# Performance work log

Measured on AMD Instinct MI355X. Metric: run time of the kernel, lower is better.

Reference implementation:

```python
import jax, jax.numpy as jnp
import numpy as np

B, L, E, H = 2, 2048, 1024, 16
HD = E // H          # head_dim = 64
G = H // 4           # heads per kernel-size group = 4


def _dwconv(x, w, b):
    """Causal depthwise conv. x: (B, G, L, D); w: (D, k); b: (D,).
    Matches PadLeft(k-1) + Conv1d(D, D, k, groups=D): y[l] = sum_j w[:, j] * x[l - (k-1) + j] + b."""
    k = w.shape[-1]
    Lx = x.shape[2]
    xp = jnp.pad(x, ((0, 0), (0, 0), (k - 1, 0), (0, 0)))
    out = b
    for j in range(k):
        out = out + xp[:, :, j:j + Lx, :] * w[:, j]
    return out


def setup_inputs() -> dict:
    key = jax.random.key(0)
    ks = jax.random.split(key, 32)
    s = 0.02
    inp = {"x": jax.random.normal(ks[0], (B, L, E), jnp.float32)}
    for i, n in enumerate(["Wq", "Wk", "Wv", "Wo"]):
        inp[n] = jax.random.normal(ks[1 + i], (E, E), jnp.float32) * s
    inp["bo"] = jax.random.normal(ks[5], (E,), jnp.float32) * s
    i = 6
    for ksz in (3, 5, 7):
        for pfx in ("q", "k", "v"):
            inp[f"{pfx}{ksz}_w"] = jax.random.normal(ks[i], (HD, ksz), jnp.float32) * (1.0 / ksz)
            inp[f"{pfx}{ksz}_b"] = jax.random.normal(ks[i + 1], (HD,), jnp.float32) * s
            i += 2
    return inp


def reference(x, Wq, Wk, Wv, Wo, bo,
              q3_w, q3_b, k3_w, k3_b, v3_w, v3_b,
              q5_w, q5_b, k5_w, k5_b, v5_w, v5_b,
              q7_w, q7_b, k7_w, k7_b, v7_w, v7_b):
    b, l, _ = x.shape

    def split(t):  # (b, l, E) -> (b, 4, G, l, HD)
        return t.reshape(b, l, 4, G, HD).transpose(0, 2, 3, 1, 4)

    q = split(x @ Wq.T)
    k = split(x @ Wk.T)
    v = split(x @ Wv.T)

    # NOTE: faithful to source quirks -- k and v convs are applied to the
    # (already convolved) q group, not to k/v.
    q0, k0, v0 = q[:, 0], k[:, 0], v[:, 0]
    q1 = _dwconv(q[:, 1], q3_w, q3_b)
    k1 = _dwconv(q1, k3_w, k3_b)
    v1 = _dwconv(q1, v3_w, v3_b)
    q2 = _dwconv(q[:, 2], q5_w, q5_b)
    k2 = _dwconv(q2, k5_w, k5_b)
    v2 = _dwconv(q2, v5_w, v5_b)
    q3 = _dwconv(q[:, 3], q7_w, q7_b)
    k3 = _dwconv(q3, k7_w, k7_b)
    v3 = _dwconv(q3, v7_w, v7_b)

    Q = jnp.concatenate([q0, q1, q2, q3], axis=1)  # (b, H, l, HD)
    K = jnp.concatenate([k0, k1, k2, k3], axis=1)
    V = jnp.concatenate([v0, v1, v2, v3], axis=1)

    logit = jnp.einsum('bnid,bnjd->bnij', Q, K) * (HD ** -0.5)
    attn = jax.nn.softmax(logit, axis=-1)
    attn_out = jnp.einsum('bnij,bnjd->bnid', attn, V)

    # Source quirk: output uses rearranged V, discarding attn_out.
    out = V.transpose(0, 2, 1, 3).reshape(b, l, E)
    # keep the attention compute alive without changing the math
    out = out + 0.0 * attn_out.transpose(0, 2, 1, 3).reshape(b, l, E)
    return out @ Wo.T + bo
```

## Files before the change

### kernel.cpp

```cpp
#include <hip/hip_runtime.h>
#include <hip/hip_bf16.h>
#include <stdint.h>

#define L_SEQ 2048
#define MTOT  4096
#define EDIM  1024

typedef __attribute__((ext_vector_type(8))) short bf16x8;
typedef __attribute__((ext_vector_type(4))) float f32x4;
typedef __attribute__((ext_vector_type(16))) float f32x16;
typedef __attribute__((ext_vector_type(4))) float float4v;
typedef __attribute__((ext_vector_type(4))) unsigned short us4;

__device__ __forceinline__ unsigned short f2b(float f) {
    union { float f; unsigned u; } v; v.f = f;
    return (unsigned short)((v.u + 0x7FFFu + ((v.u >> 16) & 1u)) >> 16);
}
__device__ __forceinline__ float b2f(unsigned short h) {
    union { unsigned u; float f; } v; v.u = ((unsigned)h) << 16;
    return v.f;
}
__device__ __forceinline__ unsigned cvtpk(float lo, float hi) {
    unsigned r;
    asm("v_cvt_pk_bf16_f32 %0, %1, %2" : "=v"(r) : "v"(lo), "v"(hi));
    return r;
}
__device__ __forceinline__ void lds16(const void* g, void* l) {
    __builtin_amdgcn_global_load_lds((const __attribute__((address_space(1))) void*)g,
                                     (__attribute__((address_space(3))) void*)l, 16, 0, 0);
}

__global__ __launch_bounds__(256) void wprep_kernel(
    const float* __restrict__ Wq, const float* __restrict__ Wv,
    const float* __restrict__ Wo,
    unsigned short* __restrict__ W1b, unsigned short* __restrict__ Wob,
    const float* __restrict__ q3w, const float* __restrict__ q3b,
    const float* __restrict__ v3w, const float* __restrict__ v3b,
    const float* __restrict__ q5w, const float* __restrict__ q5b,
    const float* __restrict__ v5w, const float* __restrict__ v5b,
    const float* __restrict__ q7w, const float* __restrict__ q7b,
    const float* __restrict__ v7w, const float* __restrict__ v7b,
    float* __restrict__ H, float* __restrict__ Beff, float* __restrict__ Corr)
{
    if (blockIdx.x >= 2048) {
        int ch = (blockIdx.x - 2048) * 256 + threadIdx.x;
        int g = ch >> 8, d = ch & 63, k = 3 + 2 * g;
        const float* qw = (g == 0) ? q3w : (g == 1) ? q5w : q7w;
        const float* qb = (g == 0) ? q3b : (g == 1) ? q5b : q7b;
        const float* vw = (g == 0) ? v3w : (g == 1) ? v5w : v7w;
        const float* vb = (g == 0) ? v3b : (g == 1) ? v5b : v7b;

        float hq[7], hv[7];
        for (int i = 0; i < 7; ++i) { hq[i] = 0.f; hv[i] = 0.f; }
        for (int i = 0; i < k; ++i) {
            hq[i] = qw[d * k + (k - 1 - i)];
            hv[i] = vw[d * k + (k - 1 - i)];
        }
        float h[13];
        for (int i = 0; i < 13; ++i) h[i] = 0.f;
        for (int a = 0; a < 7; ++a)
            for (int b = 0; b < 7; ++b)
                h[a + b] += hq[a] * hv[b];
        for (int i = 0; i < 13; ++i) H[i * 768 + ch] = h[i];

        float sv = 0.f;
        for (int j = 0; j < k; ++j) sv += vw[d * k + j];
        Beff[ch] = qb[d] * sv + vb[d];

        for (int l = 0; l < 6; ++l) {
            float s2 = 0.f;
            for (int i = l + 1; i < 7; ++i) s2 += hv[i];
            Corr[l * 768 + ch] = qb[d] * s2;
        }
        return;
    }
    const int WQ = (EDIM * EDIM) / 4;
    int i = blockIdx.x * 256 + threadIdx.x;
    const float* src;
    unsigned short* dst;
    int j;
    if (i < WQ) {
        j = i * 4;
        int row = j >> 10;
        src = (row < 256) ? Wv : Wq;
        dst = W1b;
    } else {
        j = (i - WQ) * 4; src = Wo; dst = Wob;
    }
    float4v v = *(const float4v*)(src + j);
    us4 o;
    o[0] = f2b(v[0]); o[1] = f2b(v[1]); o[2] = f2b(v[2]); o[3] = f2b(v[3]);
    *(us4*)(dst + j) = o;
}

template <int TA, int OUT_MODE>
__global__ __launch_bounds__(512, 2) void gemm_f(
    const float* __restrict__ Af,
    const unsigned short* __restrict__ Ab0, const unsigned short* __restrict__ Ab1,
    int tsplit,
    const unsigned short* __restrict__ BT,
    unsigned short* __restrict__ Cb, float* __restrict__ Cf,
    const float* __restrict__ bias)
{
    constexpr int ABUF = TA ? 49152 : 32768;
    constexpr int ABYT = TA ? 32768 : 16384;
    __shared__ uint8_t sh[3 * ABUF];

    int orig = blockIdx.y * 8 + blockIdx.x;
    int wg   = (orig & 7) * 32 + (orig >> 3);
    const int m0 = (wg >> 3) * 128, n0 = (wg & 7) * 128;

    const int tid  = threadIdx.x;
    const int wid  = tid >> 6;
    const int lane = tid & 63;
    const int wr   = wid >> 2;
    const int wc   = (wid >> 1) & 1;
    const int kh   = wid & 1;
    const int l31  = lane & 31, hi = lane >> 5;

    f32x16 acc[2][2] = {};

    auto stage = [&](int buf, int t) {
        uint8_t* Abase = sh + buf * ABUF;
        uint8_t* Bbase = Abase + ABYT;
        if (TA) {
            const float* Asrc = Af + (size_t)m0 * EDIM + t * 64;
#pragma unroll
            for (int j = 0; j < 4; ++j) {
                int slot = j * 512 + tid;
                int row = slot >> 4, c = (slot & 15) ^ (row & 15);
                lds16(Asrc + (size_t)row * EDIM + c * 4,
                      Abase + j * 8192 + wid * 1024);
            }
        } else {
            const unsigned short* Asrc =
                (t < tsplit ? Ab0 : Ab1) + (size_t)m0 * EDIM + t * 64;
#pragma unroll
            for (int j = 0; j < 2; ++j) {
                int slot = j * 512 + tid;
                int row = slot >> 3, c = (slot & 7) ^ (row & 7);
                lds16(Asrc + (size_t)row * EDIM + c * 8,
                      Abase + j * 8192 + wid * 1024);
            }
        }
        const unsigned short* Bsrc = BT + (size_t)n0 * EDIM + t * 64;
#pragma unroll
        for (int j = 0; j < 2; ++j) {
            int slot = j * 512 + tid;
            int row = slot >> 3, c = (slot & 7) ^ (row & 7);
            lds16(Bsrc + (size_t)row * EDIM + c * 8,
                  Bbase + j * 8192 + wid * 1024);
        }
    };

    auto compute = [&](int buf) {
        const uint8_t* Abase = sh + buf * ABUF;
        const unsigned short* bs = (const unsigned short*)(Abase + ABYT);
#pragma unroll
        for (int s = 0; s < 2; ++s) {
            bf16x8 a[2], b[2];
#pragma unroll
            for (int mi = 0; mi < 2; ++mi) {
                int row = wr * 64 + mi * 32 + l31;
                if (TA) {
                    const float* as = (const float*)Abase;
                    int c0 = kh * 8 + s * 4 + hi * 2;
                    f32x4 lo = *(const f32x4*)(as + row * 64 + ((c0 ^ (row & 15)) * 4));
                    f32x4 h4 = *(const f32x4*)(as + row * 64 + (((c0 + 1) ^ (row & 15)) * 4));
                    union { unsigned u[4]; bf16x8 v; } fu;
                    fu.u[0] = cvtpk(lo[0], lo[1]); fu.u[1] = cvtpk(lo[2], lo[3]);
                    fu.u[2] = cvtpk(h4[0], h4[1]); fu.u[3] = cvtpk(h4[2], h4[3]);
                    a[mi] = fu.v;
                } else {
                    const unsigned short* as = (const unsigned short*)Abase;
                    int cg = kh * 4 + s * 2 + hi;
                    a[mi] = *(const bf16x8*)(as + row * 64 + ((cg ^ (row & 7)) * 8));
                }
            }
#pragma unroll
            for (int ni = 0; ni < 2; ++ni) {
                int row = wc * 64 + ni * 32 + l31;
                int cg = kh * 4 + s * 2 + hi;
                b[ni] = *(const bf16x8*)(bs + row * 64 + ((cg ^ (row & 7)) * 8));
            }
#pragma unroll
            for (int mi = 0; mi < 2; ++mi)
#pragma unroll
                for (int ni = 0; ni < 2; ++ni)
                    acc[mi][ni] = __builtin_amdgcn_mfma_f32_32x32x16_bf16(a[mi], b[ni], acc[mi][ni], 0, 0, 0);
        }
    };

    const int NT = EDIM >> 6;
    stage(0, 0);
    stage(1, 1);
    if (TA) asm volatile("s_waitcnt vmcnt(6)" ::: "memory");
    else    asm volatile("s_waitcnt vmcnt(4)" ::: "memory");
    __builtin_amdgcn_s_barrier();
    asm volatile("" ::: "memory");

    for (int t = 0; t < NT; ++t) {
        if (t + 2 < NT) stage((t + 2) % 3, t + 2);
        compute(t % 3);
        if (t + 1 < NT) {
            if (t + 2 < NT) {
                if (TA) asm volatile("s_waitcnt vmcnt(6)" ::: "memory");
                else    asm volatile("s_waitcnt vmcnt(4)" ::: "memory");
            } else {
                asm volatile("s_waitcnt vmcnt(0)" ::: "memory");
            }
            __builtin_amdgcn_s_barrier();
            asm volatile("" ::: "memory");
        }
    }

    __syncthreads();
    float* Mg = (float*)sh;
    const int mgbase = (wr * 2 + wc) * 4096;
    if (kh) {
#pragma unroll
        for (int mi = 0; mi < 2; ++mi)
#pragma unroll
            for (int ni = 0; ni < 2; ++ni) {
                int col = ni * 32 + l31;
#pragma unroll
                for (int q = 0; q < 4; ++q) {
                    int grp = mi * 8 + 2 * q + hi;
                    int adr = mgbase + col * 64 + (((grp) ^ (col & 15)) << 2);
                    f32x4 v;
                    v[0] = acc[mi][ni][q * 4 + 0]; v[1] = acc[mi][ni][q * 4 + 1];
                    v[2] = acc[mi][ni][q * 4 + 2]; v[3] = acc[mi][ni][q * 4 + 3];
                    *(f32x4*)(Mg + adr) = v;
                }
            }
    }
    __syncthreads();
    if (!kh) {
#pragma unroll
        for (int mi = 0; mi < 2; ++mi) {
#pragma unroll
            for (int ni = 0; ni < 2; ++ni) {
                int col = ni * 32 + l31;
                int gcol = n0 + wc * 64 + col;
#pragma unroll
                for (int q = 0; q < 4; ++q) {
                    int grp = mi * 8 + 2 * q + hi;
                    int adr = mgbase + col * 64 + (((grp) ^ (col & 15)) << 2);
                    f32x4 p = *(const f32x4*)(Mg + adr);
                    int rowb = m0 + wr * 64 + mi * 32 + 8 * q + 4 * hi;
#pragma unroll
                    for (int j = 0; j < 4; ++j) {
                        float v = acc[mi][ni][q * 4 + j] + p[j];
                        if (OUT_MODE == 0) {
                            Cb[(size_t)(rowb + j) * EDIM + gcol] = f2b(v);
                        } else {
                            Cf[(size_t)(rowb + j) * EDIM + gcol] = v + bias[gcol];
                        }
                    }
                }
            }
        }
    }
}

__global__ __launch_bounds__(256) void conv_kernel(
    const unsigned short* __restrict__ T, unsigned short* __restrict__ V,
    const float* __restrict__ H, const float* __restrict__ Beff,
    const float* __restrict__ Corr)
{
    unsigned w  = blockIdx.x * 256 + threadIdx.x;
    unsigned rp = w / 192u;
    int c4 = (int)(w - rp * 192u);
    int m  = (int)rp * 2;
    int ch = c4 * 4;
    int e0 = 256 + ch;
    const unsigned short* tp = T + (size_t)m * EDIM + e0;
    unsigned short*       vp = V + (size_t)m * EDIM + e0;
    int l  = m & (L_SEQ - 1);
    float4v b4 = *(const float4v*)(Beff + ch);
    float4v acc0 = b4, acc1 = b4;

    {
        float4v h = *(const float4v*)(H + ch);
        us4 t = *(const us4*)(tp + EDIM);
        acc1[0] += h[0] * b2f(t[0]); acc1[1] += h[1] * b2f(t[1]);
        acc1[2] += h[2] * b2f(t[2]); acc1[3] += h[3] * b2f(t[3]);
    }
    int ni = (l < 12) ? l : 12;
    for (int i = 0; i <= ni; ++i) {
        us4 t = *(const us4*)(tp - (size_t)i * EDIM);
        float4v h0 = *(const float4v*)(H + i * 768 + ch);
        acc0[0] += h0[0] * b2f(t[0]); acc0[1] += h0[1] * b2f(t[1]);
        acc0[2] += h0[2] * b2f(t[2]); acc0[3] += h0[3] * b2f(t[3]);
        if (i < 12) {
            float4v h1 = *(const float4v*)(H + (i + 1) * 768 + ch);
            acc1[0] += h1[0] * b2f(t[0]); acc1[1] += h1[1] * b2f(t[1]);
            acc1[2] += h1[2] * b2f(t[2]); acc1[3] += h1[3] * b2f(t[3]);
        }
    }
    if (l < 6) {
        float4v c = *(const float4v*)(Corr + l * 768 + ch);
        acc0[0] -= c[0]; acc0[1] -= c[1]; acc0[2] -= c[2]; acc0[3] -= c[3];
    }
    if (l + 1 < 6) {
        float4v c = *(const float4v*)(Corr + (l + 1) * 768 + ch);
        acc1[0] -= c[0]; acc1[1] -= c[1]; acc1[2] -= c[2]; acc1[3] -= c[3];
    }
    us4 o0, o1;
    o0[0] = f2b(acc0[0]); o0[1] = f2b(acc0[1]); o0[2] = f2b(acc0[2]); o0[3] = f2b(acc0[3]);
    o1[0] = f2b(acc1[0]); o1[1] = f2b(acc1[1]); o1[2] = f2b(acc1[2]); o1[3] = f2b(acc1[3]);
    *(us4*)vp = o0;
    *(us4*)(vp + EDIM) = o1;
}

extern "C" void kernel_launch(void* const* d_in, const int* in_sizes, int n_in,
                              void* d_out, int out_size, void* d_ws, size_t ws_size,
                              hipStream_t stream)
{
    const float* x  = (const float*)d_in[0];
    const float* Wq = (const float*)d_in[1];
    const float* Wv = (const float*)d_in[3];
    const float* Wo = (const float*)d_in[4];
    const float* bo = (const float*)d_in[5];

    uint8_t* ws = (uint8_t*)d_ws;
    unsigned short* W1b = (unsigned short*)(ws);
    unsigned short* Wob = (unsigned short*)(ws + (2u  << 20));
    unsigned short* T   = (unsigned short*)(ws + (4u  << 20));
    unsigned short* V   = (unsigned short*)(ws + (12u << 20));
    float* H    = (float*)(ws + (20u << 20));
    float* Beff = (float*)(ws + (20u << 20) + (64u << 10));
    float* Corr = (float*)(ws + (20u << 20) + (96u << 10));

    wprep_kernel<<<2051, 256, 0, stream>>>(
        Wq, Wv, Wo, W1b, Wob,
        (const float*)d_in[6],  (const float*)d_in[7],
        (const float*)d_in[10], (const float*)d_in[11],
        (const float*)d_in[12], (const float*)d_in[13],
        (const float*)d_in[16], (const float*)d_in[17],
        (const float*)d_in[18], (const float*)d_in[19],
        (const float*)d_in[22], (const float*)d_in[23],
        H, Beff, Corr);

    dim3 gg(EDIM / 128, MTOT / 128);
    gemm_f<1, 0><<<gg, 512, 0, stream>>>(x, nullptr, nullptr, 0,
                                         W1b, T, nullptr, nullptr);

    conv_kernel<<<1536, 256, 0, stream>>>(T, V, H, Beff, Corr);

    gemm_f<0, 1><<<gg, 512, 0, stream>>>(nullptr, T, V, 4,
                                         Wob, nullptr, (float*)d_out, bo);
}
```

Baseline: 53.78 us.

## Halve GEMM K-tile to shrink LDS and raise occupancy, deepen bf16 pipeline

```diff
diff --git a/kernel.cpp b/kernel.cpp
--- a/kernel.cpp
+++ b/kernel.cpp
@@ -94,7 +94,7 @@
 }
 
 template <int TA, int OUT_MODE>
-__global__ __launch_bounds__(512, 2) void gemm_f(
+__global__ __launch_bounds__(512, 4) void gemm_f(
     const float* __restrict__ Af,
     const unsigned short* __restrict__ Ab0, const unsigned short* __restrict__ Ab1,
     int tsplit,
@@ -102,9 +102,11 @@
     unsigned short* __restrict__ Cb, float* __restrict__ Cf,
     const float* __restrict__ bias)
 {
-    constexpr int ABUF = TA ? 49152 : 32768;
-    constexpr int ABYT = TA ? 32768 : 16384;
-    __shared__ uint8_t sh[3 * ABUF];
+    constexpr int ABYT = TA ? 16384 : 8192;
+    constexpr int BBYT = 8192;
+    constexpr int BUF  = ABYT + BBYT;
+    constexpr int NBUF = TA ? 3 : 4;
+    __shared__ uint8_t sh[NBUF * BUF];
 
     int orig = blockIdx.y * 8 + blockIdx.x;
     int wg   = (orig & 7) * 32 + (orig >> 3);
@@ -121,93 +123,85 @@
     f32x16 acc[2][2] = {};
 
     auto stage = [&](int buf, int t) {
-        uint8_t* Abase = sh + buf * ABUF;
+        uint8_t* Abase = sh + buf * BUF;
         uint8_t* Bbase = Abase + ABYT;
         if (TA) {
-            const float* Asrc = Af + (size_t)m0 * EDIM + t * 64;
-#pragma unroll
-            for (int j = 0; j < 4; ++j) {
+            const float* Asrc = Af + (size_t)m0 * EDIM + t * 32;
+#pragma unroll
+            for (int j = 0; j < 2; ++j) {
                 int slot = j * 512 + tid;
-                int row = slot >> 4, c = (slot & 15) ^ (row & 15);
+                int row = slot >> 3, c = (slot & 7) ^ (row & 7);
                 lds16(Asrc + (size_t)row * EDIM + c * 4,
                       Abase + j * 8192 + wid * 1024);
             }
         } else {
             const unsigned short* Asrc =
-                (t < tsplit ? Ab0 : Ab1) + (size_t)m0 * EDIM + t * 64;
-#pragma unroll
-            for (int j = 0; j < 2; ++j) {
-                int slot = j * 512 + tid;
-                int row = slot >> 3, c = (slot & 7) ^ (row & 7);
-                lds16(Asrc + (size_t)row * EDIM + c * 8,
-                      Abase + j * 8192 + wid * 1024);
+                (t < tsplit ? Ab0 : Ab1) + (size_t)m0 * EDIM + t * 32;
+            int row = tid >> 2, c = (tid & 3) ^ (row & 3);
+            lds16(Asrc + (size_t)row * EDIM + c * 8, Abase + wid * 1024);
+        }
+        const unsigned short* Bsrc = BT + (size_t)n0 * EDIM + t * 32;
+        int row = tid >> 2, c = (tid & 3) ^ (row & 3);
+        lds16(Bsrc + (size_t)row * EDIM + c * 8, Bbase + wid * 1024);
+    };
+
+    auto compute = [&](int buf) {
+        const uint8_t* Abase = sh + buf * BUF;
+        const unsigned short* bs = (const unsigned short*)(Abase + ABYT);
+        bf16x8 a[2], b[2];
+#pragma unroll
+        for (int mi = 0; mi < 2; ++mi) {
+            int row = wr * 64 + mi * 32 + l31;
+            if (TA) {
+                const float* as = (const float*)Abase;
+                int c0 = kh * 4 + hi * 2;
+                f32x4 lo = *(const f32x4*)(as + row * 32 + ((c0 ^ (row & 7)) * 4));
+                f32x4 h4 = *(const f32x4*)(as + row * 32 + (((c0 + 1) ^ (row & 7)) * 4));
+                union { unsigned u[4]; bf16x8 v; } fu;
+                fu.u[0] = cvtpk(lo[0], lo[1]); fu.u[1] = cvtpk(lo[2], lo[3]);
+                fu.u[2] = cvtpk(h4[0], h4[1]); fu.u[3] = cvtpk(h4[2], h4[3]);
+                a[mi] = fu.v;
+            } else {
+                const unsigned short* as = (const unsigned short*)Abase;
+                int cg = kh * 2 + hi;
+                a[mi] = *(const bf16x8*)(as + row * 32 + ((cg ^ (row & 3)) * 8));
             }
         }
-        const unsigned short* Bsrc = BT + (size_t)n0 * EDIM + t * 64;
-#pragma unroll
-        for (int j = 0; j < 2; ++j) {
-            int slot = j * 512 + tid;
-            int row = slot >> 3, c = (slot & 7) ^ (row & 7);
-            lds16(Bsrc + (size_t)row * EDIM + c * 8,
-                  Bbase + j * 8192 + wid * 1024);
-        }
+#pragma unroll
+        for (int ni = 0; ni < 2; ++ni) {
+            int row = wc * 64 + ni * 32 + l31;
+            int cg = kh * 2 + hi;
+            b[ni] = *(const bf16x8*)(bs + row * 32 + ((cg ^ (row & 3)) * 8));
+        }
+#pragma unroll
+        for (int mi = 0; mi < 2; ++mi)
+#pragma unroll
+            for (int ni = 0; ni < 2; ++ni)
+                acc[mi][ni] = __builtin_amdgcn_mfma_f32_32x32x16_bf16(a[mi], b[ni], acc[mi][ni], 0, 0, 0);
     };
 
-    auto compute = [&](int buf) {
-        const uint8_t* Abase = sh + buf * ABUF;
-        const unsigned short* bs = (const unsigned short*)(Abase + ABYT);
-#pragma unroll
-        for (int s = 0; s < 2; ++s) {
-            bf16x8 a[2], b[2];
-#pragma unroll
-            for (int mi = 0; mi < 2; ++mi) {
-                int row = wr * 64 + mi * 32 + l31;
-                if (TA) {
-                    const float* as = (const float*)Abase;
-                    int c0 = kh * 8 + s * 4 + hi * 2;
-                    f32x4 lo = *(const f32x4*)(as + row * 64 + ((c0 ^ (row & 15)) * 4));
-                    f32x4 h4 = *(const f32x4*)(as + row * 64 + (((c0 + 1) ^ (row & 15)) * 4));
-                    union { unsigned u[4]; bf16x8 v; } fu;
-                    fu.u[0] = cvtpk(lo[0], lo[1]); fu.u[1] = cvtpk(lo[2], lo[3]);
-                    fu.u[2] = cvtpk(h4[0], h4[1]); fu.u[3] = cvtpk(h4[2], h4[3]);
-                    a[mi] = fu.v;
-                } else {
-                    const unsigned short* as = (const unsigned short*)Abase;
-                    int cg = kh * 4 + s * 2 + hi;
-                    a[mi] = *(const bf16x8*)(as + row * 64 + ((cg ^ (row & 7)) * 8));
-                }
-            }
-#pragma unroll
-            for (int ni = 0; ni < 2; ++ni) {
-                int row = wc * 64 + ni * 32 + l31;
-                int cg = kh * 4 + s * 2 + hi;
-                b[ni] = *(const bf16x8*)(bs + row * 64 + ((cg ^ (row & 7)) * 8));
-            }
-#pragma unroll
-            for (int mi = 0; mi < 2; ++mi)
-#pragma unroll
-                for (int ni = 0; ni < 2; ++ni)
-                    acc[mi][ni] = __builtin_amdgcn_mfma_f32_32x32x16_bf16(a[mi], b[ni], acc[mi][ni], 0, 0, 0);
-        }
-    };
-
-    const int NT = EDIM >> 6;
+    const int NT = EDIM >> 5;
+    constexpr int LPT = TA ? 3 : 2;
     stage(0, 0);
     stage(1, 1);
-    if (TA) asm volatile("s_waitcnt vmcnt(6)" ::: "memory");
+    if (!TA) stage(2, 2);
+    if (TA) asm volatile("s_waitcnt vmcnt(3)" ::: "memory");
     else    asm volatile("s_waitcnt vmcnt(4)" ::: "memory");
     __builtin_amdgcn_s_barrier();
     asm volatile("" ::: "memory");
 
     for (int t = 0; t < NT; ++t) {
-        if (t + 2 < NT) stage((t + 2) % 3, t + 2);
-        compute(t % 3);
+        constexpr int D = NBUF - 1;
+        if (t + D < NT) stage((t + D) % NBUF, t + D);
+        compute(t % NBUF);
         if (t + 1 < NT) {
-            if (t + 2 < NT) {
-                if (TA) asm volatile("s_waitcnt vmcnt(6)" ::: "memory");
-                else    asm volatile("s_waitcnt vmcnt(4)" ::: "memory");
+            if (TA) {
+                if (t + 2 < NT) asm volatile("s_waitcnt vmcnt(3)" ::: "memory");
+                else            asm volatile("s_waitcnt vmcnt(0)" ::: "memory");
             } else {
-                asm volatile("s_waitcnt vmcnt(0)" ::: "memory");
+                if (t + 3 < NT)      asm volatile("s_waitcnt vmcnt(4)" ::: "memory");
+                else if (t + 2 < NT) asm volatile("s_waitcnt vmcnt(2)" ::: "memory");
+                else                 asm volatile("s_waitcnt vmcnt(0)" ::: "memory");
             }
             __builtin_amdgcn_s_barrier();
             asm volatile("" ::: "memory");
@@ -216,50 +210,54 @@
 
     __syncthreads();
     float* Mg = (float*)sh;
-    const int mgbase = (wr * 2 + wc) * 4096;
-    if (kh) {
-#pragma unroll
-        for (int mi = 0; mi < 2; ++mi)
-#pragma unroll
-            for (int ni = 0; ni < 2; ++ni) {
-                int col = ni * 32 + l31;
-#pragma unroll
-                for (int q = 0; q < 4; ++q) {
-                    int grp = mi * 8 + 2 * q + hi;
-                    int adr = mgbase + col * 64 + (((grp) ^ (col & 15)) << 2);
-                    f32x4 v;
-                    v[0] = acc[mi][ni][q * 4 + 0]; v[1] = acc[mi][ni][q * 4 + 1];
-                    v[2] = acc[mi][ni][q * 4 + 2]; v[3] = acc[mi][ni][q * 4 + 3];
-                    *(f32x4*)(Mg + adr) = v;
+#pragma unroll
+    for (int p = 0; p < 2; ++p) {
+        const int mgbase = wc * 4096;
+        if (kh && wr == p) {
+#pragma unroll
+            for (int mi = 0; mi < 2; ++mi)
+#pragma unroll
+                for (int ni = 0; ni < 2; ++ni) {
+                    int col = ni * 32 + l31;
+#pragma unroll
+                    for (int q = 0; q < 4; ++q) {
+                        int grp = mi * 8 + 2 * q + hi;
+                        int adr = mgbase + col * 64 + (((grp) ^ (col & 15)) << 2);
+                        f32x4 v;
+                        v[0] = acc[mi][ni][q * 4 + 0]; v[1] = acc[mi][ni][q * 4 + 1];
+                        v[2] = acc[mi][ni][q * 4 + 2]; v[3] = acc[mi][ni][q * 4 + 3];
+                        *(f32x4*)(Mg + adr) = v;
+                    }
                 }
-            }
-    }
-    __syncthreads();
-    if (!kh) {
-#pragma unroll
-        for (int mi = 0; mi < 2; ++mi) {
-#pragma unroll
-            for (int ni = 0; ni < 2; ++ni) {
-                int col = ni * 32 + l31;
-                int gcol = n0 + wc * 64 + col;
-#pragma unroll
-                for (int q = 0; q < 4; ++q) {
-                    int grp = mi * 8 + 2 * q + hi;
-                    int adr = mgbase + col * 64 + (((grp) ^ (col & 15)) << 2);
-                    f32x4 p = *(const f32x4*)(Mg + adr);
-                    int rowb = m0 + wr * 64 + mi * 32 + 8 * q + 4 * hi;
-#pragma unroll
-                    for (int j = 0; j < 4; ++j) {
-                        float v = acc[mi][ni][q * 4 + j] + p[j];
-                        if (OUT_MODE == 0) {
-                            Cb[(size_t)(rowb + j) * EDIM + gcol] = f2b(v);
-                        } else {
-                            Cf[(size_t)(rowb + j) * EDIM + gcol] = v + bias[gcol];
+        }
+        __syncthreads();
+        if (!kh && wr == p) {
+#pragma unroll
+            for (int mi = 0; mi < 2; ++mi) {
+#pragma unroll
+                for (int ni = 0; ni < 2; ++ni) {
+                    int col = ni * 32 + l31;
+                    int gcol = n0 + wc * 64 + col;
+#pragma unroll
+                    for (int q = 0; q < 4; ++q) {
+                        int grp = mi * 8 + 2 * q + hi;
+                        int adr = mgbase + col * 64 + (((grp) ^ (col & 15)) << 2);
+                        f32x4 pp = *(const f32x4*)(Mg + adr);
+                        int rowb = m0 + wr * 64 + mi * 32 + 8 * q + 4 * hi;
+#pragma unroll
+                        for (int j = 0; j < 4; ++j) {
+                            float v = acc[mi][ni][q * 4 + j] + pp[j];
+                            if (OUT_MODE == 0) {
+                                Cb[(size_t)(rowb + j) * EDIM + gcol] = f2b(v);
+                            } else {
+                                Cf[(size_t)(rowb + j) * EDIM + gcol] = v + bias[gcol];
+                            }
                         }
                     }
                 }
             }
         }
+        __syncthreads();
     }
 }
 
@@ -348,6 +346,6 @@
 
     conv_kernel<<<1536, 256, 0, stream>>>(T, V, H, Beff, Corr);
 
-    gemm_f<0, 1><<<gg, 512, 0, stream>>>(nullptr, T, V, 4,
+    gemm_f<0, 1><<<gg, 512, 0, stream>>>(nullptr, T, V, 8,
                                          Wob, nullptr, (float*)d_out, bo);
 }
```

Measured after the change: 83.08 us. 54.5% more time.

## Move Wo bf16 conversion into conv kernel and deepen output GEMM pipeline

Applied to the files above, without the earlier changes.

```diff
diff --git a/kernel.cpp b/kernel.cpp
--- a/kernel.cpp
+++ b/kernel.cpp
@@ -32,8 +32,7 @@
 
 __global__ __launch_bounds__(256) void wprep_kernel(
     const float* __restrict__ Wq, const float* __restrict__ Wv,
-    const float* __restrict__ Wo,
-    unsigned short* __restrict__ W1b, unsigned short* __restrict__ Wob,
+    unsigned short* __restrict__ W1b,
     const float* __restrict__ q3w, const float* __restrict__ q3b,
     const float* __restrict__ v3w, const float* __restrict__ v3b,
     const float* __restrict__ q5w, const float* __restrict__ q5b,
@@ -42,8 +41,8 @@
     const float* __restrict__ v7w, const float* __restrict__ v7b,
     float* __restrict__ H, float* __restrict__ Beff, float* __restrict__ Corr)
 {
-    if (blockIdx.x >= 2048) {
-        int ch = (blockIdx.x - 2048) * 256 + threadIdx.x;
+    if (blockIdx.x >= 1024) {
+        int ch = (blockIdx.x - 1024) * 256 + threadIdx.x;
         int g = ch >> 8, d = ch & 63, k = 3 + 2 * g;
         const float* qw = (g == 0) ? q3w : (g == 1) ? q5w : q7w;
         const float* qb = (g == 0) ? q3b : (g == 1) ? q5b : q7b;
@@ -74,23 +73,13 @@
         }
         return;
     }
-    const int WQ = (EDIM * EDIM) / 4;
-    int i = blockIdx.x * 256 + threadIdx.x;
-    const float* src;
-    unsigned short* dst;
-    int j;
-    if (i < WQ) {
-        j = i * 4;
-        int row = j >> 10;
-        src = (row < 256) ? Wv : Wq;
-        dst = W1b;
-    } else {
-        j = (i - WQ) * 4; src = Wo; dst = Wob;
-    }
+    int j = (blockIdx.x * 256 + threadIdx.x) * 4;
+    int row = j >> 10;
+    const float* src = (row < 256) ? Wv : Wq;
     float4v v = *(const float4v*)(src + j);
     us4 o;
     o[0] = f2b(v[0]); o[1] = f2b(v[1]); o[2] = f2b(v[2]); o[3] = f2b(v[3]);
-    *(us4*)(dst + j) = o;
+    *(us4*)(W1b + j) = o;
 }
 
 template <int TA, int OUT_MODE>
@@ -104,7 +93,8 @@
 {
     constexpr int ABUF = TA ? 49152 : 32768;
     constexpr int ABYT = TA ? 32768 : 16384;
-    __shared__ uint8_t sh[3 * ABUF];
+    constexpr int NBUF = TA ? 3 : 4;
+    __shared__ uint8_t sh[NBUF * ABUF];
 
     int orig = blockIdx.y * 8 + blockIdx.x;
     int wg   = (orig & 7) * 32 + (orig >> 3);
@@ -194,20 +184,24 @@
     const int NT = EDIM >> 6;
     stage(0, 0);
     stage(1, 1);
+    if (!TA) stage(2, 2);
     if (TA) asm volatile("s_waitcnt vmcnt(6)" ::: "memory");
-    else    asm volatile("s_waitcnt vmcnt(4)" ::: "memory");
+    else    asm volatile("s_waitcnt vmcnt(8)" ::: "memory");
     __builtin_amdgcn_s_barrier();
     asm volatile("" ::: "memory");
 
     for (int t = 0; t < NT; ++t) {
-        if (t + 2 < NT) stage((t + 2) % 3, t + 2);
-        compute(t % 3);
+        constexpr int D = NBUF - 1;
+        if (t + D < NT) stage((t + D) % NBUF, t + D);
+        compute(t % NBUF);
         if (t + 1 < NT) {
-            if (t + 2 < NT) {
-                if (TA) asm volatile("s_waitcnt vmcnt(6)" ::: "memory");
-                else    asm volatile("s_waitcnt vmcnt(4)" ::: "memory");
+            if (TA) {
+                if (t + 2 < NT) asm volatile("s_waitcnt vmcnt(6)" ::: "memory");
+                else            asm volatile("s_waitcnt vmcnt(0)" ::: "memory");
             } else {
-                asm volatile("s_waitcnt vmcnt(0)" ::: "memory");
+                if (t + 3 < NT)      asm volatile("s_waitcnt vmcnt(8)" ::: "memory");
+                else if (t + 2 < NT) asm volatile("s_waitcnt vmcnt(4)" ::: "memory");
+                else                 asm volatile("s_waitcnt vmcnt(0)" ::: "memory");
             }
             __builtin_amdgcn_s_barrier();
             asm volatile("" ::: "memory");
@@ -266,8 +260,17 @@
 __global__ __launch_bounds__(256) void conv_kernel(
     const unsigned short* __restrict__ T, unsigned short* __restrict__ V,
     const float* __restrict__ H, const float* __restrict__ Beff,
-    const float* __restrict__ Corr)
+    const float* __restrict__ Corr,
+    const float* __restrict__ Wo, unsigned short* __restrict__ Wob)
 {
+    if (blockIdx.x >= 1536) {
+        int j = ((blockIdx.x - 1536) * 256 + threadIdx.x) * 4;
+        float4v v = *(const float4v*)(Wo + j);
+        us4 o;
+        o[0] = f2b(v[0]); o[1] = f2b(v[1]); o[2] = f2b(v[2]); o[3] = f2b(v[3]);
+        *(us4*)(Wob + j) = o;
+        return;
+    }
     unsigned w  = blockIdx.x * 256 + threadIdx.x;
     unsigned rp = w / 192u;
     int c4 = (int)(w - rp * 192u);
@@ -332,8 +335,8 @@
     float* Beff = (float*)(ws + (20u << 20) + (64u << 10));
     float* Corr = (float*)(ws + (20u << 20) + (96u << 10));
 
-    wprep_kernel<<<2051, 256, 0, stream>>>(
-        Wq, Wv, Wo, W1b, Wob,
+    wprep_kernel<<<1027, 256, 0, stream>>>(
+        Wq, Wv, W1b,
         (const float*)d_in[6],  (const float*)d_in[7],
         (const float*)d_in[10], (const float*)d_in[11],
         (const float*)d_in[12], (const float*)d_in[13],
@@ -346,7 +349,7 @@
     gemm_f<1, 0><<<gg, 512, 0, stream>>>(x, nullptr, nullptr, 0,
                                          W1b, T, nullptr, nullptr);
 
-    conv_kernel<<<1536, 256, 0, stream>>>(T, V, H, Beff, Corr);
+    conv_kernel<<<2560, 256, 0, stream>>>(T, V, H, Beff, Corr, Wo, Wob);
 
     gemm_f<0, 1><<<gg, 512, 0, stream>>>(nullptr, T, V, 4,
                                          Wob, nullptr, (float*)d_out, bo);
```

Result: no change. 54.19 us (+0.8%).

## Fuse causal depthwise conv into first GEMM epilogue with halo recompute

Applied to the files above, without the earlier changes.

```diff
diff --git a/kernel.cpp b/kernel.cpp
--- a/kernel.cpp
+++ b/kernel.cpp
@@ -93,22 +93,21 @@
     *(us4*)(dst + j) = o;
 }
 
-template <int TA, int OUT_MODE>
-__global__ __launch_bounds__(512, 2) void gemm_f(
-    const float* __restrict__ Af,
-    const unsigned short* __restrict__ Ab0, const unsigned short* __restrict__ Ab1,
-    int tsplit,
-    const unsigned short* __restrict__ BT,
-    unsigned short* __restrict__ Cb, float* __restrict__ Cf,
-    const float* __restrict__ bias)
+__global__ __launch_bounds__(512, 2) void gemm1_fused(
+    const float* __restrict__ Af, const unsigned short* __restrict__ BT,
+    unsigned short* __restrict__ V,
+    const float* __restrict__ H, const float* __restrict__ Beff,
+    const float* __restrict__ Corr)
 {
-    constexpr int ABUF = TA ? 49152 : 32768;
-    constexpr int ABYT = TA ? 32768 : 16384;
+    constexpr int ABUF = 49152, ABYT = 32768;
     __shared__ uint8_t sh[3 * ABUF];
 
     int orig = blockIdx.y * 8 + blockIdx.x;
     int wg   = (orig & 7) * 32 + (orig >> 3);
     const int m0 = (wg >> 3) * 128, n0 = (wg & 7) * 128;
+    const bool fir = (n0 >= 256);
+    const int  m0h = (m0 == 0) ? 0 : (m0 - 32);
+    const int  lbase = m0 & (L_SEQ - 1);
 
     const int tid  = threadIdx.x;
     const int wid  = tid >> 6;
@@ -117,43 +116,40 @@
     const int wc   = (wid >> 1) & 1;
     const int kh   = wid & 1;
     const int l31  = lane & 31, hi = lane >> 5;
+    const bool firw = fir && (wr == 0);
 
     f32x16 acc[2][2] = {};
+    f32x16 hacc[2] = {};
+
+    f32x4 h0s0a = {}, h0s0b = {}, h0s1a = {}, h0s1b = {};
+    f32x4 h1s0a = {}, h1s0b = {}, h1s1a = {}, h1s1b = {};
+    const float* hrow = Af + (size_t)(m0h + l31) * EDIM + kh * 32 + hi * 8;
+
+#define HALOLOAD(B, t) do { if (firw) {                                     \
+        const float* hp = hrow + (t) * 64;                                  \
+        h##B##s0a = *(const f32x4*)(hp);      h##B##s0b = *(const f32x4*)(hp + 4);  \
+        h##B##s1a = *(const f32x4*)(hp + 16); h##B##s1b = *(const f32x4*)(hp + 20); } } while (0)
 
     auto stage = [&](int buf, int t) {
         uint8_t* Abase = sh + buf * ABUF;
         uint8_t* Bbase = Abase + ABYT;
-        if (TA) {
-            const float* Asrc = Af + (size_t)m0 * EDIM + t * 64;
-#pragma unroll
-            for (int j = 0; j < 4; ++j) {
-                int slot = j * 512 + tid;
-                int row = slot >> 4, c = (slot & 15) ^ (row & 15);
-                lds16(Asrc + (size_t)row * EDIM + c * 4,
-                      Abase + j * 8192 + wid * 1024);
-            }
-        } else {
-            const unsigned short* Asrc =
-                (t < tsplit ? Ab0 : Ab1) + (size_t)m0 * EDIM + t * 64;
-#pragma unroll
-            for (int j = 0; j < 2; ++j) {
-                int slot = j * 512 + tid;
-                int row = slot >> 3, c = (slot & 7) ^ (row & 7);
-                lds16(Asrc + (size_t)row * EDIM + c * 8,
-                      Abase + j * 8192 + wid * 1024);
-            }
+        const float* Asrc = Af + (size_t)m0 * EDIM + t * 64;
+#pragma unroll
+        for (int j = 0; j < 4; ++j) {
+            int slot = j * 512 + tid;
+            int row = slot >> 4, c = (slot & 15) ^ (row & 15);
+            lds16(Asrc + (size_t)row * EDIM + c * 4, Abase + j * 8192 + wid * 1024);
         }
         const unsigned short* Bsrc = BT + (size_t)n0 * EDIM + t * 64;
 #pragma unroll
         for (int j = 0; j < 2; ++j) {
             int slot = j * 512 + tid;
             int row = slot >> 3, c = (slot & 7) ^ (row & 7);
-            lds16(Bsrc + (size_t)row * EDIM + c * 8,
-                  Bbase + j * 8192 + wid * 1024);
+            lds16(Bsrc + (size_t)row * EDIM + c * 8, Bbase + j * 8192 + wid * 1024);
         }
     };
 
-    auto compute = [&](int buf) {
+    auto compute = [&](int buf, f32x4 hs0a, f32x4 hs0b, f32x4 hs1a, f32x4 hs1b) {
         const uint8_t* Abase = sh + buf * ABUF;
         const unsigned short* bs = (const unsigned short*)(Abase + ABYT);
 #pragma unroll
@@ -162,20 +158,14 @@
 #pragma unroll
             for (int mi = 0; mi < 2; ++mi) {
                 int row = wr * 64 + mi * 32 + l31;
-                if (TA) {
-                    const float* as = (const float*)Abase;
-                    int c0 = kh * 8 + s * 4 + hi * 2;
-                    f32x4 lo = *(const f32x4*)(as + row * 64 + ((c0 ^ (row & 15)) * 4));
-                    f32x4 h4 = *(const f32x4*)(as + row * 64 + (((c0 + 1) ^ (row & 15)) * 4));
-                    union { unsigned u[4]; bf16x8 v; } fu;
-                    fu.u[0] = cvtpk(lo[0], lo[1]); fu.u[1] = cvtpk(lo[2], lo[3]);
-                    fu.u[2] = cvtpk(h4[0], h4[1]); fu.u[3] = cvtpk(h4[2], h4[3]);
-                    a[mi] = fu.v;
-                } else {
-                    const unsigned short* as = (const unsigned short*)Abase;
-                    int cg = kh * 4 + s * 2 + hi;
-                    a[mi] = *(const bf16x8*)(as + row * 64 + ((cg ^ (row & 7)) * 8));
-                }
+                const float* as = (const float*)Abase;
+                int c0 = kh * 8 + s * 4 + hi * 2;
+                f32x4 lo = *(const f32x4*)(as + row * 64 + ((c0 ^ (row & 15)) * 4));
+                f32x4 h4 = *(const f32x4*)(as + row * 64 + (((c0 + 1) ^ (row & 15)) * 4));
+                union { unsigned u[4]; bf16x8 v; } fu;
+                fu.u[0] = cvtpk(lo[0], lo[1]); fu.u[1] = cvtpk(lo[2], lo[3]);
+                fu.u[2] = cvtpk(h4[0], h4[1]); fu.u[3] = cvtpk(h4[2], h4[3]);
+                a[mi] = fu.v;
             }
 #pragma unroll
             for (int ni = 0; ni < 2; ++ni) {
@@ -188,31 +178,44 @@
 #pragma unroll
                 for (int ni = 0; ni < 2; ++ni)
                     acc[mi][ni] = __builtin_amdgcn_mfma_f32_32x32x16_bf16(a[mi], b[ni], acc[mi][ni], 0, 0, 0);
+            if (firw) {
+                f32x4 pa = s ? hs1a : hs0a, pb = s ? hs1b : hs0b;
+                union { unsigned u[4]; bf16x8 v; } hu;
+                hu.u[0] = cvtpk(pa[0], pa[1]); hu.u[1] = cvtpk(pa[2], pa[3]);
+                hu.u[2] = cvtpk(pb[0], pb[1]); hu.u[3] = cvtpk(pb[2], pb[3]);
+                hacc[0] = __builtin_amdgcn_mfma_f32_32x32x16_bf16(hu.v, b[0], hacc[0], 0, 0, 0);
+                hacc[1] = __builtin_amdgcn_mfma_f32_32x32x16_bf16(hu.v, b[1], hacc[1], 0, 0, 0);
+            }
         }
     };
 
     const int NT = EDIM >> 6;
+    HALOLOAD(0, 0);
     stage(0, 0);
     stage(1, 1);
-    if (TA) asm volatile("s_waitcnt vmcnt(6)" ::: "memory");
-    else    asm volatile("s_waitcnt vmcnt(4)" ::: "memory");
+    asm volatile("s_waitcnt vmcnt(6)" ::: "memory");
     __builtin_amdgcn_s_barrier();
     asm volatile("" ::: "memory");
 
-    for (int t = 0; t < NT; ++t) {
-        if (t + 2 < NT) stage((t + 2) % 3, t + 2);
-        compute(t % 3);
-        if (t + 1 < NT) {
-            if (t + 2 < NT) {
-                if (TA) asm volatile("s_waitcnt vmcnt(6)" ::: "memory");
-                else    asm volatile("s_waitcnt vmcnt(4)" ::: "memory");
-            } else {
-                asm volatile("s_waitcnt vmcnt(0)" ::: "memory");
-            }
+    for (int tt = 0; tt < NT; tt += 2) {
+        HALOLOAD(1, tt + 1);
+        if (tt + 2 < NT) stage((tt + 2) % 3, tt + 2);
+        compute(tt % 3, h0s0a, h0s0b, h0s1a, h0s1b);
+        if (tt + 2 < NT) asm volatile("s_waitcnt vmcnt(6)" ::: "memory");
+        else             asm volatile("s_waitcnt vmcnt(0)" ::: "memory");
+        __builtin_amdgcn_s_barrier();
+        asm volatile("" ::: "memory");
+        if (tt + 2 < NT) HALOLOAD(0, tt + 2);
+        if (tt + 3 < NT) stage((tt + 3) % 3, tt + 3);
+        compute((tt + 1) % 3, h1s0a, h1s0b, h1s1a, h1s1b);
+        if (tt + 2 < NT) {
+            if (tt + 3 < NT) asm volatile("s_waitcnt vmcnt(6)" ::: "memory");
+            else             asm volatile("s_waitcnt vmcnt(0)" ::: "memory");
             __builtin_amdgcn_s_barrier();
             asm volatile("" ::: "memory");
         }
     }
+#undef HALOLOAD
 
     __syncthreads();
     float* Mg = (float*)sh;
@@ -233,6 +236,219 @@
                     *(f32x4*)(Mg + adr) = v;
                 }
             }
+        if (firw) {
+#pragma unroll
+            for (int ni = 0; ni < 2; ++ni) {
+                int hcol = ni * 32 + l31;
+#pragma unroll
+                for (int q = 0; q < 4; ++q) {
+                    int hg = 2 * q + hi;
+                    int adr = 16384 + wc * 2048 + hcol * 32 + ((hg ^ (hcol & 7)) << 2);
+                    f32x4 v;
+                    v[0] = hacc[ni][q * 4 + 0]; v[1] = hacc[ni][q * 4 + 1];
+                    v[2] = hacc[ni][q * 4 + 2]; v[3] = hacc[ni][q * 4 + 3];
+                    *(f32x4*)(Mg + adr) = v;
+                }
+            }
+        }
+    }
+    __syncthreads();
+    if (fir) {
+        unsigned short* Tl = (unsigned short*)(sh + 81920);
+        if (!kh) {
+#pragma unroll
+            for (int mi = 0; mi < 2; ++mi)
+#pragma unroll
+                for (int ni = 0; ni < 2; ++ni) {
+                    int col = wc * 64 + ni * 32 + l31;
+#pragma unroll
+                    for (int q = 0; q < 4; ++q) {
+                        int grp = mi * 8 + 2 * q + hi;
+                        int adr = mgbase + (ni * 32 + l31) * 64 + (((grp) ^ ((ni * 32 + l31) & 15)) << 2);
+                        f32x4 p = *(const f32x4*)(Mg + adr);
+                        int Lr = 32 + wr * 64 + mi * 32 + 8 * q + 4 * hi;
+                        us4 o;
+#pragma unroll
+                        for (int j = 0; j < 4; ++j) o[j] = f2b(acc[mi][ni][q * 4 + j] + p[j]);
+                        *(us4*)(Tl + col * 172 + Lr) = o;
+                    }
+                }
+            if (wr == 0) {
+#pragma unroll
+                for (int ni = 0; ni < 2; ++ni) {
+                    int hcol = ni * 32 + l31;
+                    int col = wc * 64 + hcol;
+#pragma unroll
+                    for (int q = 0; q < 4; ++q) {
+                        int hg = 2 * q + hi;
+                        int adr = 16384 + wc * 2048 + hcol * 32 + ((hg ^ (hcol & 7)) << 2);
+                        f32x4 p = *(const f32x4*)(Mg + adr);
+                        int Lr = 8 * q + 4 * hi;
+                        us4 o;
+#pragma unroll
+                        for (int j = 0; j < 4; ++j) o[j] = f2b(hacc[ni][q * 4 + j] + p[j]);
+                        *(us4*)(Tl + col * 172 + Lr) = o;
+                    }
+                }
+            }
+        }
+        __syncthreads();
+        int c = tid & 127, rb = tid >> 7;
+        int ch = n0 + c - 256;
+        float h[13];
+#pragma unroll
+        for (int i = 0; i < 13; ++i) h[i] = H[i * 768 + ch];
+        float beff = Beff[ch];
+        const unsigned short* wp = Tl + c * 172 + 20 + rb * 32;
+        float wf[44];
+#pragma unroll
+        for (int j = 0; j < 11; ++j) {
+            us4 t4 = *(const us4*)(wp + j * 4);
+            wf[j * 4 + 0] = b2f(t4[0]); wf[j * 4 + 1] = b2f(t4[1]);
+            wf[j * 4 + 2] = b2f(t4[2]); wf[j * 4 + 3] = b2f(t4[3]);
+        }
+        if (lbase == 0 && rb == 0) {
+#pragma unroll
+            for (int j = 0; j < 12; ++j) wf[j] = 0.f;
+        }
+        unsigned short* vp = V + (size_t)(m0 + rb * 32) * EDIM + n0 + c;
+#pragma unroll
+        for (int rr = 0; rr < 32; ++rr) {
+            float s = beff;
+#pragma unroll
+            for (int i = 0; i < 13; ++i) s += h[i] * wf[12 + rr - i];
+            int l = lbase + rb * 32 + rr;
+            if (l < 6) s -= Corr[l * 768 + ch];
+            vp[(size_t)rr * EDIM] = f2b(s);
+        }
+    } else {
+        if (!kh) {
+#pragma unroll
+            for (int mi = 0; mi < 2; ++mi) {
+#pragma unroll
+                for (int ni = 0; ni < 2; ++ni) {
+                    int col = ni * 32 + l31;
+                    int gcol = n0 + wc * 64 + col;
+#pragma unroll
+                    for (int q = 0; q < 4; ++q) {
+                        int grp = mi * 8 + 2 * q + hi;
+                        int adr = mgbase + col * 64 + (((grp) ^ (col & 15)) << 2);
+                        f32x4 p = *(const f32x4*)(Mg + adr);
+                        int rowb = m0 + wr * 64 + mi * 32 + 8 * q + 4 * hi;
+#pragma unroll
+                        for (int j = 0; j < 4; ++j)
+                            V[(size_t)(rowb + j) * EDIM + gcol] = f2b(acc[mi][ni][q * 4 + j] + p[j]);
+                    }
+                }
+            }
+        }
+    }
+}
+
+__global__ __launch_bounds__(512, 2) void gemm2_k(
+    const unsigned short* __restrict__ Ab, const unsigned short* __restrict__ BT,
+    float* __restrict__ Cf, const float* __restrict__ bias)
+{
+    constexpr int ABUF = 32768, ABYT = 16384;
+    __shared__ uint8_t sh[3 * ABUF];
+
+    int orig = blockIdx.y * 8 + blockIdx.x;
+    int wg   = (orig & 7) * 32 + (orig >> 3);
+    const int m0 = (wg >> 3) * 128, n0 = (wg & 7) * 128;
+
+    const int tid  = threadIdx.x;
+    const int wid  = tid >> 6;
+    const int lane = tid & 63;
+    const int wr   = wid >> 2;
+    const int wc   = (wid >> 1) & 1;
+    const int kh   = wid & 1;
+    const int l31  = lane & 31, hi = lane >> 5;
+
+    f32x16 acc[2][2] = {};
+
+    auto stage = [&](int buf, int t) {
+        uint8_t* Abase = sh + buf * ABUF;
+        uint8_t* Bbase = Abase + ABYT;
+        const unsigned short* Asrc = Ab + (size_t)m0 * EDIM + t * 64;
+#pragma unroll
+        for (int j = 0; j < 2; ++j) {
+            int slot = j * 512 + tid;
+            int row = slot >> 3, c = (slot & 7) ^ (row & 7);
+            lds16(Asrc + (size_t)row * EDIM + c * 8, Abase + j * 8192 + wid * 1024);
+        }
+        const unsigned short* Bsrc = BT + (size_t)n0 * EDIM + t * 64;
+#pragma unroll
+        for (int j = 0; j < 2; ++j) {
+            int slot = j * 512 + tid;
+            int row = slot >> 3, c = (slot & 7) ^ (row & 7);
+            lds16(Bsrc + (size_t)row * EDIM + c * 8, Bbase + j * 8192 + wid * 1024);
+        }
+    };
+
+    auto compute = [&](int buf) {
+        const uint8_t* Abase = sh + buf * ABUF;
+        const unsigned short* as = (const unsigned short*)Abase;
+        const unsigned short* bs = (const unsigned short*)(Abase + ABYT);
+#pragma unroll
+        for (int s = 0; s < 2; ++s) {
+            bf16x8 a[2], b[2];
+#pragma unroll
+            for (int mi = 0; mi < 2; ++mi) {
+                int row = wr * 64 + mi * 32 + l31;
+                int cg = kh * 4 + s * 2 + hi;
+                a[mi] = *(const bf16x8*)(as + row * 64 + ((cg ^ (row & 7)) * 8));
+            }
+#pragma unroll
+            for (int ni = 0; ni < 2; ++ni) {
+                int row = wc * 64 + ni * 32 + l31;
+                int cg = kh * 4 + s * 2 + hi;
+                b[ni] = *(const bf16x8*)(bs + row * 64 + ((cg ^ (row & 7)) * 8));
+            }
+#pragma unroll
+            for (int mi = 0; mi < 2; ++mi)
+#pragma unroll
+                for (int ni = 0; ni < 2; ++ni)
+                    acc[mi][ni] = __builtin_amdgcn_mfma_f32_32x32x16_bf16(a[mi], b[ni], acc[mi][ni], 0, 0, 0);
+        }
+    };
+
+    const int NT = EDIM >> 6;
+    stage(0, 0);
+    stage(1, 1);
+    asm volatile("s_waitcnt vmcnt(4)" ::: "memory");
+    __builtin_amdgcn_s_barrier();
+    asm volatile("" ::: "memory");
+
+    for (int t = 0; t < NT; ++t) {
+        if (t + 2 < NT) stage((t + 2) % 3, t + 2);
+        compute(t % 3);
+        if (t + 1 < NT) {
+            if (t + 2 < NT) asm volatile("s_waitcnt vmcnt(4)" ::: "memory");
+            else            asm volatile("s_waitcnt vmcnt(0)" ::: "memory");
+            __builtin_amdgcn_s_barrier();
+            asm volatile("" ::: "memory");
+        }
+    }
+
+    __syncthreads();
+    float* Mg = (float*)sh;
+    const int mgbase = (wr * 2 + wc) * 4096;
+    if (kh) {
+#pragma unroll
+        for (int mi = 0; mi < 2; ++mi)
+#pragma unroll
+            for (int ni = 0; ni < 2; ++ni) {
+                int col = ni * 32 + l31;
+#pragma unroll
+                for (int q = 0; q < 4; ++q) {
+                    int grp = mi * 8 + 2 * q + hi;
+                    int adr = mgbase + col * 64 + (((grp) ^ (col & 15)) << 2);
+                    f32x4 v;
+                    v[0] = acc[mi][ni][q * 4 + 0]; v[1] = acc[mi][ni][q * 4 + 1];
+                    v[2] = acc[mi][ni][q * 4 + 2]; v[3] = acc[mi][ni][q * 4 + 3];
+                    *(f32x4*)(Mg + adr) = v;
+                }
+            }
     }
     __syncthreads();
     if (!kh) {
@@ -249,68 +465,12 @@
                     f32x4 p = *(const f32x4*)(Mg + adr);
                     int rowb = m0 + wr * 64 + mi * 32 + 8 * q + 4 * hi;
 #pragma unroll
-                    for (int j = 0; j < 4; ++j) {
-                        float v = acc[mi][ni][q * 4 + j] + p[j];
-                        if (OUT_MODE == 0) {
-                            Cb[(size_t)(rowb + j) * EDIM + gcol] = f2b(v);
-                        } else {
-                            Cf[(size_t)(rowb + j) * EDIM + gcol] = v + bias[gcol];
-                        }
-                    }
-                }
-            }
-        }
-    }
-}
-
-__global__ __launch_bounds__(256) void conv_kernel(
-    const unsigned short* __restrict__ T, unsigned short* __restrict__ V,
-    const float* __restrict__ H, const float* __restrict__ Beff,
-    const float* __restrict__ Corr)
-{
-    unsigned w  = blockIdx.x * 256 + threadIdx.x;
-    unsigned rp = w / 192u;
-    int c4 = (int)(w - rp * 192u);
-    int m  = (int)rp * 2;
-    int ch = c4 * 4;
-    int e0 = 256 + ch;
-    const unsigned short* tp = T + (size_t)m * EDIM + e0;
-    unsigned short*       vp = V + (size_t)m * EDIM + e0;
-    int l  = m & (L_SEQ - 1);
-    float4v b4 = *(const float4v*)(Beff + ch);
-    float4v acc0 = b4, acc1 = b4;
-
-    {
-        float4v h = *(const float4v*)(H + ch);
-        us4 t = *(const us4*)(tp + EDIM);
-        acc1[0] += h[0] * b2f(t[0]); acc1[1] += h[1] * b2f(t[1]);
-        acc1[2] += h[2] * b2f(t[2]); acc1[3] += h[3] * b2f(t[3]);
-    }
-    int ni = (l < 12) ? l : 12;
-    for (int i = 0; i <= ni; ++i) {
-        us4 t = *(const us4*)(tp - (size_t)i * EDIM);
-        float4v h0 = *(const float4v*)(H + i * 768 + ch);
-        acc0[0] += h0[0] * b2f(t[0]); acc0[1] += h0[1] * b2f(t[1]);
-        acc0[2] += h0[2] * b2f(t[2]); acc0[3] += h0[3] * b2f(t[3]);
-        if (i < 12) {
-            float4v h1 = *(const float4v*)(H + (i + 1) * 768 + ch);
-            acc1[0] += h1[0] * b2f(t[0]); acc1[1] += h1[1] * b2f(t[1]);
-            acc1[2] += h1[2] * b2f(t[2]); acc1[3] += h1[3] * b2f(t[3]);
-        }
-    }
-    if (l < 6) {
-        float4v c = *(const float4v*)(Corr + l * 768 + ch);
-        acc0[0] -= c[0]; acc0[1] -= c[1]; acc0[2] -= c[2]; acc0[3] -= c[3];
-    }
-    if (l + 1 < 6) {
-        float4v c = *(const float4v*)(Corr + (l + 1) * 768 + ch);
-        acc1[0] -= c[0]; acc1[1] -= c[1]; acc1[2] -= c[2]; acc1[3] -= c[3];
-    }
-    us4 o0, o1;
-    o0[0] = f2b(acc0[0]); o0[1] = f2b(acc0[1]); o0[2] = f2b(acc0[2]); o0[3] = f2b(acc0[3]);
-    o1[0] = f2b(acc1[0]); o1[1] = f2b(acc1[1]); o1[2] = f2b(acc1[2]); o1[3] = f2b(acc1[3]);
-    *(us4*)vp = o0;
-    *(us4*)(vp + EDIM) = o1;
+                    for (int j = 0; j < 4; ++j)
+                        Cf[(size_t)(rowb + j) * EDIM + gcol] = acc[mi][ni][q * 4 + j] + p[j] + bias[gcol];
+                }
+            }
+        }
+    }
 }
 
 extern "C" void kernel_launch(void* const* d_in, const int* in_sizes, int n_in,
@@ -326,11 +486,10 @@
     uint8_t* ws = (uint8_t*)d_ws;
     unsigned short* W1b = (unsigned short*)(ws);
     unsigned short* Wob = (unsigned short*)(ws + (2u  << 20));
-    unsigned short* T   = (unsigned short*)(ws + (4u  << 20));
-    unsigned short* V   = (unsigned short*)(ws + (12u << 20));
-    float* H    = (float*)(ws + (20u << 20));
-    float* Beff = (float*)(ws + (20u << 20) + (64u << 10));
-    float* Corr = (float*)(ws + (20u << 20) + (96u << 10));
+    unsigned short* V   = (unsigned short*)(ws + (4u  << 20));
+    float* H    = (float*)(ws + (12u << 20));
+    float* Beff = (float*)(ws + (12u << 20) + (64u << 10));
+    float* Corr = (float*)(ws + (12u << 20) + (96u << 10));
 
     wprep_kernel<<<2051, 256, 0, stream>>>(
         Wq, Wv, Wo, W1b, Wob,
@@ -343,11 +502,7 @@
         H, Beff, Corr);
 
     dim3 gg(EDIM / 128, MTOT / 128);
-    gemm_f<1, 0><<<gg, 512, 0, stream>>>(x, nullptr, nullptr, 0,
-                                         W1b, T, nullptr, nullptr);
-
-    conv_kernel<<<1536, 256, 0, stream>>>(T, V, H, Beff, Corr);
-
-    gemm_f<0, 1><<<gg, 512, 0, stream>>>(nullptr, T, V, 4,
-                                         Wob, nullptr, (float*)d_out, bo);
-}
+    gemm1_fused<<<gg, 512, 0, stream>>>(x, W1b, V, H, Beff, Corr);
+
+    gemm2_k<<<gg, 512, 0, stream>>>(V, Wob, (float*)d_out, bo);
+}
```

Result: no change. 53.85 us (+0.1%).
